# Kernel optimization log

Hardware: AMD Instinct MI355X
Metric: run time of the kernel (lower is better)

Reference implementation:

```python
import jax, jax.numpy as jnp
import numpy as np

L, B, S, D, H, FF, V = 4, 2, 1024, 768, 12, 3072, 50257
HD = D // H  # 64
EPS = 1e-5


def _ln(x, w, b):
    m = jnp.mean(x, axis=-1, keepdims=True)
    v = jnp.mean(jnp.square(x - m), axis=-1, keepdims=True)
    return (x - m) * jax.lax.rsqrt(v + EPS) * w + b


def setup_inputs() -> dict:
    key = jax.random.key(0)
    ks = jax.random.split(key, 8)
    std = 0.02
    inp = {
        'input_ids': jax.random.randint(ks[0], (B, S), 0, V),
        'tok_emb': jax.random.normal(ks[1], (V, D), jnp.float32) * std,
        'pos_emb': jax.random.normal(ks[2], (S, D), jnp.float32) * std,
        'ln1_w': jnp.ones((L, D), jnp.float32),
        'ln1_b': jnp.zeros((L, D), jnp.float32),
        'qkv_w': jax.random.normal(ks[3], (L, 3 * D, D), jnp.float32) * std,
        'qkv_b': jnp.zeros((L, 3 * D), jnp.float32),
        'out_w': jax.random.normal(ks[4], (L, D, D), jnp.float32) * std,
        'out_b': jnp.zeros((L, D), jnp.float32),
        'ln2_w': jnp.ones((L, D), jnp.float32),
        'ln2_b': jnp.zeros((L, D), jnp.float32),
        'fc1_w': jax.random.normal(ks[5], (L, FF, D), jnp.float32) * std,
        'fc1_b': jnp.zeros((L, FF), jnp.float32),
        'fc2_w': jax.random.normal(ks[6], (L, D, FF), jnp.float32) * std,
        'fc2_b': jnp.zeros((L, D), jnp.float32),
        'lnf_w': jnp.ones((D,), jnp.float32),
        'lnf_b': jnp.zeros((D,), jnp.float32),
    }
    return inp


def _gpt_forward(input_ids, tok_emb, pos_emb, ln1_w, ln1_b, qkv_w, qkv_b,
                 out_w, out_b, ln2_w, ln2_b, fc1_w, fc1_b, fc2_w, fc2_b,
                 lnf_w, lnf_b):
    x = tok_emb[input_ids] + pos_emb[None, :S, :]  # [B,S,D]
    causal = jnp.tril(jnp.ones((S, S), bool))  # [S,S]
    scale = 1.0 / np.sqrt(HD)
    for l in range(L):
        # --- attention ---
        h = _ln(x, ln1_w[l], ln1_b[l])
        qkv = h @ qkv_w[l].T + qkv_b[l]  # [B,S,3D]
        qkv = qkv.reshape(B, S, 3, H, HD).transpose(2, 0, 3, 1, 4)
        q, k, v = qkv[0], qkv[1], qkv[2]  # [B,H,S,HD]
        scores = jnp.einsum('bhqd,bhkd->bhqk', q, k) * scale
        scores = jnp.where(causal, scores, -jnp.inf)
        w = jax.nn.softmax(scores, axis=-1)
        a = jnp.einsum('bhqk,bhkd->bhqd', w, v)  # [B,H,S,HD]
        a = a.transpose(0, 2, 1, 3).reshape(B, S, D)
        x = x + a @ out_w[l].T + out_b[l]
        # --- ffn ---
        h = _ln(x, ln2_w[l], ln2_b[l])
        h = jax.nn.gelu(h @ fc1_w[l].T + fc1_b[l], approximate=False)
        x = x + h @ fc2_w[l].T + fc2_b[l]
    x = _ln(x, lnf_w, lnf_b)
    logits = x @ tok_emb.T  # tied lm_head, no bias
    return logits


def reference(input_ids, tok_emb, pos_emb, ln1_w, ln1_b, qkv_w, qkv_b,
              out_w, out_b, ln2_w, ln2_b, fc1_w, fc1_b, fc2_w, fc2_b,
              lnf_w, lnf_b):
    return _gpt_forward(input_ids, tok_emb, pos_emb, ln1_w, ln1_b, qkv_w,
                        qkv_b, out_w, out_b, ln2_w, ln2_b, fc1_w, fc1_b,
                        fc2_w, fc2_b, lnf_w, lnf_b)
```

## Files before the change

kernel.cpp:

```cpp
#include <hip/hip_runtime.h>
#include <cstdint>
#include <cstddef>

#define D_MODEL 768
#define NHEAD   12
#define SEQ     1024
#define NTOK    2048
#define FFDIM   3072
#define NLAYER  4
#define VOCAB   50257
#define QKVD    2304

typedef float f32x4 __attribute__((ext_vector_type(4)));
typedef __bf16 bf16x8 __attribute__((ext_vector_type(8)));

__device__ __forceinline__ unsigned short f2bf(float f) {
  unsigned int u = __float_as_uint(f);
  return (unsigned short)((u + 0x7FFFu + ((u >> 16) & 1u)) >> 16);
}

__global__ __launch_bounds__(256) void k_cvt(const float* __restrict__ in,
                                             unsigned short* __restrict__ out, int n8) {
  int i = blockIdx.x * 256 + threadIdx.x;
  if (i >= n8) return;
  const float4* p = (const float4*)in;
  float4 a = p[2 * i], b = p[2 * i + 1];
  union { unsigned short u[8]; uint4 v; } r;
  r.u[0] = f2bf(a.x); r.u[1] = f2bf(a.y); r.u[2] = f2bf(a.z); r.u[3] = f2bf(a.w);
  r.u[4] = f2bf(b.x); r.u[5] = f2bf(b.y); r.u[6] = f2bf(b.z); r.u[7] = f2bf(b.w);
  ((uint4*)out)[i] = r.v;
}

__global__ __launch_bounds__(256) void k_embed(const int* __restrict__ ids,
                                               const float* __restrict__ tok,
                                               const float* __restrict__ pos,
                                               float* __restrict__ x) {
  int gid = blockIdx.x * 256 + threadIdx.x;
  int t = gid / 192, f = gid - t * 192;
  int id = ids[t];
  float4 a = ((const float4*)tok)[(size_t)id * 192 + f];
  float4 b = ((const float4*)pos)[(size_t)(t & (SEQ - 1)) * 192 + f];
  float4 o; o.x = a.x + b.x; o.y = a.y + b.y; o.z = a.z + b.z; o.w = a.w + b.w;
  ((float4*)x)[gid] = o;
}

__global__ __launch_bounds__(256) void k_ln(const float* __restrict__ x,
                                            const float* __restrict__ w,
                                            const float* __restrict__ b,
                                            unsigned short* __restrict__ out) {
  __shared__ float red[256];
  int row = blockIdx.x, tid = threadIdx.x;
  const float* xr = x + (size_t)row * D_MODEL;
  float v0 = xr[tid], v1 = xr[tid + 256], v2 = xr[tid + 512];
  red[tid] = v0 + v1 + v2;
  __syncthreads();
  for (int o = 128; o > 0; o >>= 1) { if (tid < o) red[tid] += red[tid + o]; __syncthreads(); }
  float mean = red[0] * (1.0f / 768.0f);
  __syncthreads();
  float d0 = v0 - mean, d1 = v1 - mean, d2 = v2 - mean;
  red[tid] = d0 * d0 + d1 * d1 + d2 * d2;
  __syncthreads();
  for (int o = 128; o > 0; o >>= 1) { if (tid < o) red[tid] += red[tid + o]; __syncthreads(); }
  float rstd = rsqrtf(red[0] * (1.0f / 768.0f) + 1e-5f);
  unsigned short* orow = out + (size_t)row * D_MODEL;
  orow[tid]       = f2bf(d0 * rstd * w[tid]       + b[tid]);
  orow[tid + 256] = f2bf(d1 * rstd * w[tid + 256] + b[tid + 256]);
  orow[tid + 512] = f2bf(d2 * rstd * w[tid + 512] + b[tid + 512]);
}

__global__ __launch_bounds__(256) void k_vt(const unsigned short* __restrict__ qkv,
                                            unsigned short* __restrict__ vt) {
  __shared__ unsigned short t[64][80];
  int bid = blockIdx.x;
  int st = bid & 15, h = (bid >> 4) % NHEAD, b = bid / (16 * NHEAD);
  int tid = threadIdx.x;
  int r = tid >> 2, cq = (tid & 3) * 16;
  const unsigned short* src =
      qkv + (size_t)(b * SEQ + st * 64 + r) * QKVD + 2 * D_MODEL + h * 64 + cq;
  *(uint4*)&t[r][cq] = *(const uint4*)src;
  *(uint4*)&t[r][cq + 8] = *(const uint4*)(src + 8);
  __syncthreads();
  int d = r, j0 = cq;
  unsigned short* dst = vt + ((size_t)(b * D_MODEL) + h * 64 + d) * SEQ + st * 64 + j0;
  union { unsigned short u[8]; uint4 v; } o0, o1;
  #pragma unroll
  for (int jj = 0; jj < 8; ++jj) o0.u[jj] = t[j0 + jj][d];
  #pragma unroll
  for (int jj = 0; jj < 8; ++jj) o1.u[jj] = t[j0 + 8 + jj][d];
  *(uint4*)dst = o0.v;
  *(uint4*)(dst + 8) = o1.v;
}

__global__ __launch_bounds__(64) void k_attn(const unsigned short* __restrict__ qkv,
                                             const unsigned short* __restrict__ vt,
                                             unsigned short* __restrict__ attO) {
  int bid = blockIdx.x;
  int qt = (SEQ / 16 - 1) - (bid & 63);
  int h = (bid >> 6) % NHEAD;
  int b = bid / (64 * NHEAD);
  int lane = threadIdx.x;
  int fr = lane & 15, fq = lane >> 4;
  int qb = qt * 16;

  size_t rowQ = (size_t)(b * SEQ + qb + fr) * QKVD + h * 64;
  bf16x8 bq0 = *(const bf16x8*)(qkv + rowQ + fq * 8);
  bf16x8 bq1 = *(const bf16x8*)(qkv + rowQ + 32 + fq * 8);

  float m = -1e30f, ll = 0.0f;
  f32x4 o[4] = {};
  int nkt = (qt >> 1) + 1;
  size_t kvrow0 = (size_t)(b * SEQ) * QKVD;
  const unsigned short* vbase0 = vt + ((size_t)(b * D_MODEL) + h * 64 + fr) * SEQ;

  for (int kt = 0; kt < nkt; ++kt) {
    int kvb = kt * 32;
    bool diag = (kt == nkt - 1);
    float p[2][4];
    float tm = -1e30f;
    #pragma unroll
    for (int t = 0; t < 2; ++t) {
      size_t rowK = kvrow0 + (size_t)(kvb + t * 16 + fr) * QKVD + D_MODEL + h * 64;
      bf16x8 ak0 = *(const bf16x8*)(qkv + rowK + fq * 8);
      bf16x8 ak1 = *(const bf16x8*)(qkv + rowK + 32 + fq * 8);
      f32x4 st = {};
      st = __builtin_amdgcn_mfma_f32_16x16x32_bf16(ak0, bq0, st, 0, 0, 0);
      st = __builtin_amdgcn_mfma_f32_16x16x32_bf16(ak1, bq1, st, 0, 0, 0);
      #pragma unroll
      for (int j = 0; j < 4; ++j) {
        float s = st[j] * 0.125f;
        if (diag && (kvb + t * 16 + fq * 4 + j > qb + fr)) s = -1e30f;
        p[t][j] = s;
        tm = fmaxf(tm, s);
      }
    }
    tm = fmaxf(tm, __shfl_xor(tm, 16));
    tm = fmaxf(tm, __shfl_xor(tm, 32));
    float mnew = fmaxf(m, tm);
    float corr = __expf(m - mnew);
    float psum = 0.0f;
    #pragma unroll
    for (int t = 0; t < 2; ++t)
      #pragma unroll
      for (int j = 0; j < 4; ++j) { float e = __expf(p[t][j] - mnew); p[t][j] = e; psum += e; }
    psum += __shfl_xor(psum, 16);
    psum += __shfl_xor(psum, 32);
    ll = ll * corr + psum;
    m = mnew;
    #pragma unroll
    for (int dg = 0; dg < 4; ++dg) {
      o[dg][0] *= corr; o[dg][1] *= corr; o[dg][2] *= corr; o[dg][3] *= corr;
    }
    unsigned int lo0 = (unsigned)f2bf(p[0][0]) | ((unsigned)f2bf(p[0][1]) << 16);
    unsigned int hi0 = (unsigned)f2bf(p[0][2]) | ((unsigned)f2bf(p[0][3]) << 16);
    unsigned int lo1 = (unsigned)f2bf(p[1][0]) | ((unsigned)f2bf(p[1][1]) << 16);
    unsigned int hi1 = (unsigned)f2bf(p[1][2]) | ((unsigned)f2bf(p[1][3]) << 16);
    int sA = fr + 16 * ((fq & 1) * 2);
    int sB = sA + 16;
    unsigned int w0a = __shfl(lo0, sA), w0b = __shfl(lo1, sA);
    unsigned int w1a = __shfl(hi0, sA), w1b = __shfl(hi1, sA);
    unsigned int w2a = __shfl(lo0, sB), w2b = __shfl(lo1, sB);
    unsigned int w3a = __shfl(hi0, sB), w3b = __shfl(hi1, sB);
    bool t1 = (fq >> 1) != 0;
    uint4 pw;
    pw.x = t1 ? w0b : w0a;
    pw.y = t1 ? w1b : w1a;
    pw.z = t1 ? w2b : w2a;
    pw.w = t1 ? w3b : w3a;
    bf16x8 pb = __builtin_bit_cast(bf16x8, pw);
    const unsigned short* vp = vbase0 + kvb + fq * 8;
    #pragma unroll
    for (int dg = 0; dg < 4; ++dg) {
      bf16x8 va = *(const bf16x8*)(vp + (size_t)dg * 16 * SEQ);
      o[dg] = __builtin_amdgcn_mfma_f32_16x16x32_bf16(va, pb, o[dg], 0, 0, 0);
    }
  }
  float inv = 1.0f / ll;
  size_t obase = (size_t)(b * SEQ + qb + fr) * D_MODEL + h * 64;
  #pragma unroll
  for (int dg = 0; dg < 4; ++dg)
    #pragma unroll
    for (int j = 0; j < 4; ++j)
      attO[obase + dg * 16 + fq * 4 + j] = f2bf(o[dg][j] * inv);
}

template<int HAS_BIAS, int DO_GELU, int HAS_RES, int OUT_BF16>
__global__ __launch_bounds__(256) void k_gemm(const unsigned short* __restrict__ A,
                                              const unsigned short* __restrict__ W,
                                              const float* __restrict__ bias,
                                              const float* __restrict__ res,
                                              void* __restrict__ Cout,
                                              int N, int K) {
  __shared__ __align__(1024) unsigned short As[128 * 64];
  __shared__ __align__(1024) unsigned short Ws[128 * 64];
  int tid = threadIdx.x, lane = tid & 63, wv = tid >> 6;
  int fr = lane & 15, fq = lane >> 4;
  int wm = wv >> 1, wn = wv & 1;

  int cpx = gridDim.x >> 3;
  int id = (blockIdx.x & 7) * cpx + (blockIdx.x >> 3);
  int bm = (id & 15) * 128;
  int bn = (id >> 4) * 128;

  const unsigned short* pA[4];
  const unsigned short* pW[4];
  unsigned short* ldsA[4];
  unsigned short* ldsW[4];
  #pragma unroll
  for (int i = 0; i < 4; ++i) {
    int c = wv * 4 + i;
    int r = c * 8 + (lane >> 3);
    int up = (lane & 7) ^ (r & 7);
    pA[i] = A + (size_t)(bm + r) * K + up * 8;
    int wr = bn + r; if (wr > N - 1) wr = N - 1;
    pW[i] = W + (size_t)wr * K + up * 8;
    ldsA[i] = &As[c * 512];
    ldsW[i] = &Ws[c * 512];
  }

  const unsigned short* aB = As + (wm * 64 + fr) * 64;
  const unsigned short* wB = Ws + (wn * 64 + fr) * 64;
  int sz = fr & 7;
  int u0 = (fq ^ sz) * 8;
  int u1 = ((4 + fq) ^ sz) * 8;

  f32x4 acc[4][4] = {};

  for (int k0 = 0; k0 < K; k0 += 64) {
    #pragma unroll
    for (int i = 0; i < 4; ++i) {
      __builtin_amdgcn_global_load_lds(
          (const __attribute__((address_space(1))) unsigned int*)(pA[i] + k0),
          (__attribute__((address_space(3))) unsigned int*)ldsA[i], 16, 0, 0);
      __builtin_amdgcn_global_load_lds(
          (const __attribute__((address_space(1))) unsigned int*)(pW[i] + k0),
          (__attribute__((address_space(3))) unsigned int*)ldsW[i], 16, 0, 0);
    }
    __syncthreads();

    bf16x8 af[4][2], bf[4][2];
    #pragma unroll
    for (int mm = 0; mm < 4; ++mm) {
      af[mm][0] = *(const bf16x8*)(aB + mm * 1024 + u0);
      af[mm][1] = *(const bf16x8*)(aB + mm * 1024 + u1);
    }
    #pragma unroll
    for (int nn = 0; nn < 4; ++nn) {
      bf[nn][0] = *(const bf16x8*)(wB + nn * 1024 + u0);
      bf[nn][1] = *(const bf16x8*)(wB + nn * 1024 + u1);
    }
    #pragma unroll
    for (int mm = 0; mm < 4; ++mm)
      #pragma unroll
      for (int nn = 0; nn < 4; ++nn) {
        acc[mm][nn] = __builtin_amdgcn_mfma_f32_16x16x32_bf16(af[mm][0], bf[nn][0], acc[mm][nn], 0, 0, 0);
        acc[mm][nn] = __builtin_amdgcn_mfma_f32_16x16x32_bf16(af[mm][1], bf[nn][1], acc[mm][nn], 0, 0, 0);
      }
    __syncthreads();
  }

  #pragma unroll
  for (int nn = 0; nn < 4; ++nn) {
    int col = bn + wn * 64 + nn * 16 + fr;
    if (col >= N) continue;
    float bv = HAS_BIAS ? bias[col] : 0.0f;
    #pragma unroll
    for (int mm = 0; mm < 4; ++mm) {
      #pragma unroll
      for (int j = 0; j < 4; ++j) {
        int row = bm + wm * 64 + mm * 16 + fq * 4 + j;
        size_t idx = (size_t)row * N + col;
        float v = acc[mm][nn][j] + bv;
        if (DO_GELU) v = 0.5f * v * (1.0f + erff(v * 0.70710678118f));
        if (HAS_RES) v += res[idx];
        if (OUT_BF16) ((unsigned short*)Cout)[idx] = f2bf(v);
        else          ((float*)Cout)[idx] = v;
      }
    }
  }
}

extern "C" void kernel_launch(void* const* d_in, const int* in_sizes, int n_in,
                              void* d_out, int out_size, void* d_ws, size_t ws_size,
                              hipStream_t stream) {
  const int*   ids    = (const int*)d_in[0];
  const float* tok    = (const float*)d_in[1];
  const float* pos    = (const float*)d_in[2];
  const float* ln1_w  = (const float*)d_in[3];
  const float* ln1_b  = (const float*)d_in[4];
  const float* qkv_w  = (const float*)d_in[5];
  const float* qkv_b  = (const float*)d_in[6];
  const float* out_w  = (const float*)d_in[7];
  const float* out_b  = (const float*)d_in[8];
  const float* ln2_w  = (const float*)d_in[9];
  const float* ln2_b  = (const float*)d_in[10];
  const float* fc1_w  = (const float*)d_in[11];
  const float* fc1_b  = (const float*)d_in[12];
  const float* fc2_w  = (const float*)d_in[13];
  const float* fc2_b  = (const float*)d_in[14];
  const float* lnf_w  = (const float*)d_in[15];
  const float* lnf_b  = (const float*)d_in[16];

  char* ws = (char*)d_ws;
  float*          x    = (float*)(ws);
  unsigned short* qkvb = (unsigned short*)(ws + 6291456);
  unsigned short* h    = (unsigned short*)(ws + 15728640);
  unsigned short* attO = (unsigned short*)(ws + 18874368);
  unsigned short* gbuf = (unsigned short*)(ws + 22020096);
  unsigned short* wq   = (unsigned short*)(ws + 34603008);
  unsigned short* wo   = (unsigned short*)(ws + 48758784);
  unsigned short* w1   = (unsigned short*)(ws + 53477376);
  unsigned short* w2   = (unsigned short*)(ws + 72351744);
  unsigned short* wtok = (unsigned short*)(ws + 91226112);
  float* logits = (float*)d_out;

  {
    int n8;
    n8 = NLAYER * QKVD * D_MODEL / 8;
    k_cvt<<<(n8 + 255) / 256, 256, 0, stream>>>(qkv_w, wq, n8);
    n8 = NLAYER * D_MODEL * D_MODEL / 8;
    k_cvt<<<(n8 + 255) / 256, 256, 0, stream>>>(out_w, wo, n8);
    n8 = NLAYER * FFDIM * D_MODEL / 8;
    k_cvt<<<(n8 + 255) / 256, 256, 0, stream>>>(fc1_w, w1, n8);
    k_cvt<<<(n8 + 255) / 256, 256, 0, stream>>>(fc2_w, w2, n8);
    n8 = VOCAB * D_MODEL / 8;
    k_cvt<<<(n8 + 255) / 256, 256, 0, stream>>>(tok, wtok, n8);
  }

  k_embed<<<NTOK * 192 / 256, 256, 0, stream>>>(ids, tok, pos, x);

  for (int l = 0; l < NLAYER; ++l) {
    k_ln<<<NTOK, 256, 0, stream>>>(x, ln1_w + l * D_MODEL, ln1_b + l * D_MODEL, h);
    k_gemm<1, 0, 0, 1><<<16 * (QKVD / 128), 256, 0, stream>>>(
        h, wq + (size_t)l * QKVD * D_MODEL, qkv_b + l * QKVD, nullptr, qkvb, QKVD, D_MODEL);
    k_vt<<<2 * NHEAD * 16, 256, 0, stream>>>(qkvb, h);
    k_attn<<<2 * NHEAD * (SEQ / 16), 64, 0, stream>>>(qkvb, h, attO);
    k_gemm<1, 0, 1, 0><<<16 * (D_MODEL / 128), 256, 0, stream>>>(
        attO, wo + (size_t)l * D_MODEL * D_MODEL, out_b + l * D_MODEL, x, x, D_MODEL, D_MODEL);
    k_ln<<<NTOK, 256, 0, stream>>>(x, ln2_w + l * D_MODEL, ln2_b + l * D_MODEL, h);
    k_gemm<1, 1, 0, 1><<<16 * (FFDIM / 128), 256, 0, stream>>>(
        h, w1 + (size_t)l * FFDIM * D_MODEL, fc1_b + l * FFDIM, nullptr, gbuf, FFDIM, D_MODEL);
    k_gemm<1, 0, 1, 0><<<16 * (D_MODEL / 128), 256, 0, stream>>>(
        gbuf, w2 + (size_t)l * D_MODEL * FFDIM, fc2_b + l * D_MODEL, x, x, D_MODEL, FFDIM);
  }

  k_ln<<<NTOK, 256, 0, stream>>>(x, lnf_w, lnf_b, h);
  k_gemm<0, 0, 0, 0><<<16 * ((VOCAB + 127) / 128), 256, 0, stream>>>(
      h, wtok, nullptr, nullptr, logits, VOCAB, D_MODEL);
}
```

Measured before the change: 1.202 ms.

## Add pipelined 256x256 LM-head GEMM and merge weight conversions into one launch

Replaces the generic GEMM for the tied LM head with a dedicated 512-thread kernel. It uses 256x256 tiles, direct global-to-LDS loads into double-buffered swizzled shared memory, staged prefetch interleaved with MFMA phases, priority hints, and an XCD-aware block remap. Separately, the five fp32-to-bf16 weight conversion launches are merged into one kernel that dispatches on offset. The aim is more reuse and better load/compute overlap for the largest GEMM, plus less launch overhead. The cost is a complex hand-scheduled pipeline whose waitcnt and barrier logic must be exactly right, and full-occupancy tiles over a 50257-wide N with a clamped edge.

After: 1.269 ms. 1.06x slower.

```diff
diff --git a/kernel.cpp b/kernel.cpp
--- a/kernel.cpp
+++ b/kernel.cpp
@@ -19,16 +19,23 @@
   return (unsigned short)((u + 0x7FFFu + ((u >> 16) & 1u)) >> 16);
 }
 
-__global__ __launch_bounds__(256) void k_cvt(const float* __restrict__ in,
-                                             unsigned short* __restrict__ out, int n8) {
-  int i = blockIdx.x * 256 + threadIdx.x;
-  if (i >= n8) return;
-  const float4* p = (const float4*)in;
-  float4 a = p[2 * i], b = p[2 * i + 1];
+__global__ __launch_bounds__(256) void k_cvt5(const float* __restrict__ s0, unsigned short* __restrict__ d0, int n0,
+                                              const float* __restrict__ s1, unsigned short* __restrict__ d1, int n1,
+                                              const float* __restrict__ s2, unsigned short* __restrict__ d2, int n2,
+                                              const float* __restrict__ s3, unsigned short* __restrict__ d3, int n3,
+                                              const float* __restrict__ s4, unsigned short* __restrict__ d4, int n4) {
+  int off = blockIdx.x * 256 + threadIdx.x;
+  const float* s; unsigned short* d;
+  if (off < n0) { s = s0; d = d0; }
+  else { off -= n0; if (off < n1) { s = s1; d = d1; }
+  else { off -= n1; if (off < n2) { s = s2; d = d2; }
+  else { off -= n2; if (off < n3) { s = s3; d = d3; }
+  else { off -= n3; if (off >= n4) return; s = s4; d = d4; } } } }
+  float4 a = ((const float4*)s)[2 * off], b = ((const float4*)s)[2 * off + 1];
   union { unsigned short u[8]; uint4 v; } r;
   r.u[0] = f2bf(a.x); r.u[1] = f2bf(a.y); r.u[2] = f2bf(a.z); r.u[3] = f2bf(a.w);
   r.u[4] = f2bf(b.x); r.u[5] = f2bf(b.y); r.u[6] = f2bf(b.z); r.u[7] = f2bf(b.w);
-  ((uint4*)out)[i] = r.v;
+  ((uint4*)d)[off] = r.v;
 }
 
 __global__ __launch_bounds__(256) void k_embed(const int* __restrict__ ids,
@@ -279,6 +286,163 @@
   }
 }
 
+#define GLL16(srcp, ldsp) __builtin_amdgcn_global_load_lds( \
+    (const __attribute__((address_space(1))) unsigned int*)(srcp), \
+    (__attribute__((address_space(3))) unsigned int*)(ldsp), 16, 0, 0)
+#define STAGE_A(h, t) do { \
+  GLL16(srcA[h][0] + (size_t)(t) * 64, &LA[(t) & 1][h][ch0 * 512]); \
+  GLL16(srcA[h][1] + (size_t)(t) * 64, &LA[(t) & 1][h][ch1 * 512]); } while (0)
+#define STAGE_B(h, t) do { \
+  GLL16(srcB[h][0] + (size_t)(t) * 64, &LB[(t) & 1][h][ch0 * 512]); \
+  GLL16(srcB[h][1] + (size_t)(t) * 64, &LB[(t) & 1][h][ch1 * 512]); } while (0)
+#define MFMA16(d, a, b) __builtin_amdgcn_mfma_f32_16x16x32_bf16(a, b, d, 0, 0, 0)
+
+__global__ __launch_bounds__(512, 1) void k_lmhead(const unsigned short* __restrict__ A,
+                                                   const unsigned short* __restrict__ W,
+                                                   float* __restrict__ C,
+                                                   int N, int K) {
+  __shared__ __align__(1024) unsigned short LA[2][2][128 * 64];
+  __shared__ __align__(1024) unsigned short LB[2][2][128 * 64];
+  const int tid = threadIdx.x, lane = tid & 63, wv = tid >> 6;
+  const int fr = lane & 15, fq = lane >> 4;
+  const int wm = wv >> 2, wn = wv & 3;
+
+  int cpx = gridDim.x >> 3;
+  int id = ((int)blockIdx.x & 7) * cpx + ((int)blockIdx.x >> 3);
+  int bm = (id & 7) * 256;
+  int bn = (id >> 3) * 256;
+
+  const int ch0 = wv * 2, ch1 = wv * 2 + 1;
+  const int sr0 = ch0 * 8 + (lane >> 3);
+  const int sr1 = ch1 * 8 + (lane >> 3);
+  const int su0 = (lane & 7) ^ (sr0 & 7);
+  const int su1 = (lane & 7) ^ (sr1 & 7);
+  const unsigned short* srcA[2][2];
+  const unsigned short* srcB[2][2];
+  #pragma unroll
+  for (int h = 0; h < 2; ++h) {
+    srcA[h][0] = A + (size_t)(bm + h * 128 + sr0) * K + su0 * 8;
+    srcA[h][1] = A + (size_t)(bm + h * 128 + sr1) * K + su1 * 8;
+    int w0 = bn + h * 128 + sr0; if (w0 > N - 1) w0 = N - 1;
+    int w1 = bn + h * 128 + sr1; if (w1 > N - 1) w1 = N - 1;
+    srcB[h][0] = W + (size_t)w0 * K + su0 * 8;
+    srcB[h][1] = W + (size_t)w1 * K + su1 * 8;
+  }
+
+  const int sz = fr & 7;
+  const int u0 = (fq ^ sz) * 8;
+  const int u1 = ((4 + fq) ^ sz) * 8;
+  const int brow = (wn & 1) * 64;
+  const int hB = wn >> 1;
+
+  f32x4 acc[8][4] = {};
+  const int NT = K >> 6;
+
+  STAGE_A(0, 0); STAGE_A(1, 0); STAGE_B(0, 0); STAGE_B(1, 0);
+  STAGE_B(0, 1); STAGE_B(1, 1);
+  asm volatile("s_waitcnt vmcnt(4)" ::: "memory");
+  __builtin_amdgcn_s_barrier();
+
+  for (int kt = 0; kt < NT; ++kt) {
+    const int d = kt & 1;
+    const unsigned short* LAp = &LA[d][wm][0];
+    const unsigned short* LBp = &LB[d][hB][0];
+    bf16x8 af[4][2], bf0[2][2], bf1[2][2];
+
+    #pragma unroll
+    for (int mm = 0; mm < 4; ++mm) {
+      af[mm][0] = *(const bf16x8*)(LAp + (mm * 16 + fr) * 64 + u0);
+      af[mm][1] = *(const bf16x8*)(LAp + (mm * 16 + fr) * 64 + u1);
+    }
+    #pragma unroll
+    for (int nn = 0; nn < 2; ++nn) {
+      bf0[nn][0] = *(const bf16x8*)(LBp + (brow + nn * 16 + fr) * 64 + u0);
+      bf0[nn][1] = *(const bf16x8*)(LBp + (brow + nn * 16 + fr) * 64 + u1);
+    }
+    if (kt + 1 < NT) STAGE_A(0, kt + 1);
+    __builtin_amdgcn_s_barrier();
+    asm volatile("s_waitcnt lgkmcnt(0)" ::: "memory");
+    __builtin_amdgcn_s_setprio(1);
+    #pragma unroll
+    for (int mm = 0; mm < 4; ++mm)
+      #pragma unroll
+      for (int nn = 0; nn < 2; ++nn) {
+        acc[mm][nn] = MFMA16(acc[mm][nn], af[mm][0], bf0[nn][0]);
+        acc[mm][nn] = MFMA16(acc[mm][nn], af[mm][1], bf0[nn][1]);
+      }
+    __builtin_amdgcn_s_setprio(0);
+    __builtin_amdgcn_s_barrier();
+
+    #pragma unroll
+    for (int nn = 0; nn < 2; ++nn) {
+      bf1[nn][0] = *(const bf16x8*)(LBp + (brow + 32 + nn * 16 + fr) * 64 + u0);
+      bf1[nn][1] = *(const bf16x8*)(LBp + (brow + 32 + nn * 16 + fr) * 64 + u1);
+    }
+    if (kt + 1 < NT) STAGE_A(1, kt + 1);
+    __builtin_amdgcn_s_barrier();
+    asm volatile("s_waitcnt lgkmcnt(0)" ::: "memory");
+    __builtin_amdgcn_s_setprio(1);
+    #pragma unroll
+    for (int mm = 0; mm < 4; ++mm)
+      #pragma unroll
+      for (int nn = 0; nn < 2; ++nn) {
+        acc[mm][2 + nn] = MFMA16(acc[mm][2 + nn], af[mm][0], bf1[nn][0]);
+        acc[mm][2 + nn] = MFMA16(acc[mm][2 + nn], af[mm][1], bf1[nn][1]);
+      }
+    __builtin_amdgcn_s_setprio(0);
+    __builtin_amdgcn_s_barrier();
+
+    #pragma unroll
+    for (int mm = 0; mm < 4; ++mm) {
+      af[mm][0] = *(const bf16x8*)(LAp + (64 + mm * 16 + fr) * 64 + u0);
+      af[mm][1] = *(const bf16x8*)(LAp + (64 + mm * 16 + fr) * 64 + u1);
+    }
+    if (kt + 2 < NT) STAGE_B(0, kt + 2);
+    __builtin_amdgcn_s_barrier();
+    asm volatile("s_waitcnt lgkmcnt(0)" ::: "memory");
+    __builtin_amdgcn_s_setprio(1);
+    #pragma unroll
+    for (int mm = 0; mm < 4; ++mm)
+      #pragma unroll
+      for (int nn = 0; nn < 2; ++nn) {
+        acc[4 + mm][2 + nn] = MFMA16(acc[4 + mm][2 + nn], af[mm][0], bf1[nn][0]);
+        acc[4 + mm][2 + nn] = MFMA16(acc[4 + mm][2 + nn], af[mm][1], bf1[nn][1]);
+      }
+    __builtin_amdgcn_s_setprio(0);
+    __builtin_amdgcn_s_barrier();
+
+    if (kt + 2 < NT) STAGE_B(1, kt + 2);
+    if (kt < NT - 2) asm volatile("s_waitcnt vmcnt(4)" ::: "memory");
+    else             asm volatile("s_waitcnt vmcnt(0)" ::: "memory");
+    __builtin_amdgcn_s_barrier();
+    __builtin_amdgcn_s_setprio(1);
+    #pragma unroll
+    for (int mm = 0; mm < 4; ++mm)
+      #pragma unroll
+      for (int nn = 0; nn < 2; ++nn) {
+        acc[4 + mm][nn] = MFMA16(acc[4 + mm][nn], af[mm][0], bf0[nn][0]);
+        acc[4 + mm][nn] = MFMA16(acc[4 + mm][nn], af[mm][1], bf0[nn][1]);
+      }
+    __builtin_amdgcn_s_setprio(0);
+    __builtin_amdgcn_s_barrier();
+  }
+
+  #pragma unroll
+  for (int n = 0; n < 4; ++n) {
+    int col = bn + wn * 64 + n * 16 + fr;
+    if (col >= N) continue;
+    #pragma unroll
+    for (int m = 0; m < 8; ++m) {
+      int row = bm + wm * 128 + m * 16 + fq * 4;
+      float* cp = C + (size_t)row * N + col;
+      cp[0] = acc[m][n][0];
+      cp[(size_t)N] = acc[m][n][1];
+      cp[(size_t)2 * N] = acc[m][n][2];
+      cp[(size_t)3 * N] = acc[m][n][3];
+    }
+  }
+}
+
 extern "C" void kernel_launch(void* const* d_in, const int* in_sizes, int n_in,
                               void* d_out, int out_size, void* d_ws, size_t ws_size,
                               hipStream_t stream) {
@@ -314,16 +478,14 @@
   float* logits = (float*)d_out;
 
   {
-    int n8;
-    n8 = NLAYER * QKVD * D_MODEL / 8;
-    k_cvt<<<(n8 + 255) / 256, 256, 0, stream>>>(qkv_w, wq, n8);
-    n8 = NLAYER * D_MODEL * D_MODEL / 8;
-    k_cvt<<<(n8 + 255) / 256, 256, 0, stream>>>(out_w, wo, n8);
-    n8 = NLAYER * FFDIM * D_MODEL / 8;
-    k_cvt<<<(n8 + 255) / 256, 256, 0, stream>>>(fc1_w, w1, n8);
-    k_cvt<<<(n8 + 255) / 256, 256, 0, stream>>>(fc2_w, w2, n8);
-    n8 = VOCAB * D_MODEL / 8;
-    k_cvt<<<(n8 + 255) / 256, 256, 0, stream>>>(tok, wtok, n8);
+    int n0 = NLAYER * QKVD * D_MODEL / 8;
+    int n1 = NLAYER * D_MODEL * D_MODEL / 8;
+    int n2 = NLAYER * FFDIM * D_MODEL / 8;
+    int n3 = n2;
+    int n4 = VOCAB * D_MODEL / 8;
+    int tot = n0 + n1 + n2 + n3 + n4;
+    k_cvt5<<<(tot + 255) / 256, 256, 0, stream>>>(
+        qkv_w, wq, n0, out_w, wo, n1, fc1_w, w1, n2, fc2_w, w2, n3, tok, wtok, n4);
   }
 
   k_embed<<<NTOK * 192 / 256, 256, 0, stream>>>(ids, tok, pos, x);
@@ -344,6 +506,5 @@
   }
 
   k_ln<<<NTOK, 256, 0, stream>>>(x, lnf_w, lnf_b, h);
-  k_gemm<0, 0, 0, 0><<<16 * ((VOCAB + 127) / 128), 256, 0, stream>>>(
-      h, wtok, nullptr, nullptr, logits, VOCAB, D_MODEL);
-}
+  k_lmhead<<<8 * ((VOCAB + 255) / 256), 512, 0, stream>>>(h, wtok, logits, VOCAB, D_MODEL);
+}
```
